# Optimization experiments

Measured on AMD Instinct MI355X. Metric: run time of the kernel, lower is better.

## Reference

```python
import jax, jax.numpy as jnp
import numpy as np

COORD = 5.0
NOOBJ = 0.5
S = 14
B = 2
C = 20
BATCH = 4096


def setup_inputs() -> dict:
    key = jax.random.key(0)
    k1, k2, k3 = jax.random.split(key, 3)
    inp = jax.random.uniform(k1, (BATCH, S, S, 5 * B + C), dtype=jnp.float32)
    tgt = jax.random.uniform(k2, (BATCH, S, S, 5 * B + C), dtype=jnp.float32)
    # target confidence channels must be exactly 0/1 for the obj test
    conf = (jax.random.uniform(k3, (BATCH, S, S, B)) < 0.2).astype(jnp.float32)
    tgt = tgt.at[..., :B].set(conf)
    return {"input": inp, "target": tgt}


def reference(input, target) -> jnp.ndarray:
    n = input.shape[0]
    conf_p = input[..., :B]                      # [N,S,S,B]
    conf_t = target[..., :B]
    box_p = input[..., B:5 * B].reshape(*input.shape[:-1], B, 4)   # [N,S,S,B,4]
    box_t = target[..., B:5 * B].reshape(*target.shape[:-1], B, 4)
    cls_p = input[..., 5 * B:]                   # [N,S,S,C]
    cls_t = target[..., 5 * B:]

    obj = conf_t == 1.0                          # [N,S,S,B]
    has_obj = jnp.any(obj, axis=-1)              # [N,S,S]
    # first responsible box per cell (the original breaks at first k with obj==1)
    first = obj & (jnp.cumsum(obj.astype(jnp.int32), axis=-1) == 1)  # [N,S,S,B]
    firstf = first.astype(input.dtype)

    sq_xy = jnp.sum((box_p[..., :2] - box_t[..., :2]) ** 2, axis=-1)               # [N,S,S,B]
    sq_wh = jnp.sum((jnp.sqrt(box_p[..., 2:]) - jnp.sqrt(box_t[..., 2:])) ** 2, axis=-1)
    sq_conf = (conf_p - conf_t) ** 2                                               # [N,S,S,B]

    loss_xy = jnp.sum(firstf * sq_xy)
    loss_wh = jnp.sum(firstf * sq_wh)
    loss_objc = jnp.sum(firstf * sq_conf)
    # class loss counted once per cell containing an object
    loss_cls = jnp.sum(has_obj.astype(input.dtype) * jnp.sum((cls_p - cls_t) ** 2, axis=-1))
    # no-object: all B confidences in cells with no responsible box
    noobj_mask = (~has_obj).astype(input.dtype)[..., None]
    loss_noobjc = jnp.sum(noobj_mask * sq_conf)

    total = COORD * (loss_xy + loss_wh) + NOOBJ * loss_noobjc + loss_objc + loss_cls
    return total / n
```

## Files before the change

### kernel.cpp

```cpp
#include <hip/hip_runtime.h>


#define COORD 5.0f
#define NOOBJ 0.5f

#define NCELLS   (4096 * 14 * 14)
#define CPC      128
#define CHB      (CPC * 120)
#define NCHUNKS  (NCELLS / CPC)
#define GRID     512
#define THREADS  128

__device__ __forceinline__ float d2f(float a, float b) { float d = a - b; return d * d; }
__device__ __forceinline__ float sqd(float a, float b) {
    return a + b - 2.0f * sqrtf(a * b);
}

__global__ __launch_bounds__(THREADS) void yolo_loss_kernel(
    const float* __restrict__ inp,
    const float* __restrict__ tgt,
    float* __restrict__ out,
    float inv_n)
{
    __shared__ __align__(16) char smem[2][2][CHB];
    __shared__ float wsum[2];

    const int tid  = threadIdx.x;
    const int lane = tid & 63;
    const int wid  = tid >> 6;

    const char* gsrc0 = (const char*)(wid == 0 ? inp : tgt) + (size_t)lane * 16;

    auto stage = [&](int b, int c) {
        const char* g = gsrc0 + (size_t)c * CHB;
        char* l = &smem[b][wid][0];
#pragma unroll
        for (int k = 0; k < 15; ++k) {
            __builtin_amdgcn_global_load_lds(
                (const __attribute__((address_space(1))) void*)(g + k * 1024),
                (__attribute__((address_space(3))) void*)(l + k * 1024), 16, 0, 0);
        }
    };

    float acc = 0.0f;
    int c = blockIdx.x;
    stage(0, c);
    int buf = 0;

    const int half = lane & 1;

    for (; c < NCHUNKS; c += GRID) {
        const int cn = c + GRID;
        if (cn < NCHUNKS) {
            stage(buf ^ 1, cn);
            asm volatile("s_waitcnt vmcnt(15)" ::: "memory");
        } else {
            asm volatile("s_waitcnt vmcnt(0)" ::: "memory");
        }
        asm volatile("s_barrier" ::: "memory");

        const float* li = (const float*)&smem[buf][0][0];
        const float* lt = (const float*)&smem[buf][1][0];

#pragma unroll
        for (int pass = 0; pass < 2; ++pass) {
            const int p = (lane >> 1) + 32 * pass + 64 * wid;
            const int base = 15 * lane + 960 * pass + 1920 * wid;
            const float* ip = li + base;
            const float* tp = lt + base;

            float t0 = lt[p * 30];
            float t1 = lt[p * 30 + 1];
            bool o0 = (t0 == 1.0f), o1 = (t1 == 1.0f);
            float f0 = o0 ? 1.0f : 0.0f;
            float f1 = (o1 && !o0) ? 1.0f : 0.0f;
            float h  = (o0 || o1) ? 1.0f : 0.0f;
            float nf = 1.0f - h;

            if (half == 0) {
                float s0  = d2f(ip[0], tp[0]);
                float s1  = d2f(ip[1], tp[1]);
                float xy0 = d2f(ip[2], tp[2]) + d2f(ip[3], tp[3]);
                float wh0 = sqd(ip[4], tp[4]) + sqd(ip[5], tp[5]);
                float xy1 = d2f(ip[6], tp[6]) + d2f(ip[7], tp[7]);
                float wh1 = sqd(ip[8], tp[8]) + sqd(ip[9], tp[9]);
                float cls = d2f(ip[10], tp[10]) + d2f(ip[11], tp[11]) + d2f(ip[12], tp[12])
                          + d2f(ip[13], tp[13]) + d2f(ip[14], tp[14]);
                acc += COORD * (f0 * (xy0 + wh0) + f1 * (xy1 + wh1))
                     + f0 * s0 + f1 * s1
                     + NOOBJ * nf * (s0 + s1)
                     + h * cls;
            } else {
                float cls = 0.0f;
#pragma unroll
                for (int j = 0; j < 15; ++j)
                    cls += d2f(ip[j], tp[j]);
                acc += h * cls;
            }
        }

        asm volatile("s_barrier" ::: "memory");
        buf ^= 1;
    }

#pragma unroll
    for (int off = 32; off > 0; off >>= 1)
        acc += __shfl_down(acc, off, 64);
    if (lane == 0) wsum[wid] = acc;
    __syncthreads();
    if (tid == 0) atomicAdd(out, (wsum[0] + wsum[1]) * inv_n);
}

extern "C" void kernel_launch(void* const* d_in, const int* in_sizes, int n_in,
                              void* d_out, int out_size, void* d_ws, size_t ws_size,
                              hipStream_t stream) {
    const float* inp = (const float*)d_in[0];
    const float* tgt = (const float*)d_in[1];
    float* out = (float*)d_out;

    hipMemsetAsync(out, 0, sizeof(float), stream);
    yolo_loss_kernel<<<GRID, THREADS, 0, stream>>>(inp, tgt, out, 1.0f / 4096.0f);
}
```

Before: 44.98 us.

## Give each wave its own triple-buffer-free chunk stream with two-deep prefetch and no barriers

```diff
diff --git a/kernel.cpp b/kernel.cpp
--- a/kernel.cpp
+++ b/kernel.cpp
@@ -8,64 +8,69 @@
 #define CPC      128
 #define CHB      (CPC * 120)
 #define NCHUNKS  (NCELLS / CPC)
-#define GRID     512
-#define THREADS  128
+#define NSTREAM  512
 
 __device__ __forceinline__ float d2f(float a, float b) { float d = a - b; return d * d; }
 __device__ __forceinline__ float sqd(float a, float b) {
     return a + b - 2.0f * sqrtf(a * b);
 }
 
-__global__ __launch_bounds__(THREADS) void yolo_loss_kernel(
+__global__ __launch_bounds__(128) void yolo_loss_kernel(
     const float* __restrict__ inp,
     const float* __restrict__ tgt,
     float* __restrict__ out,
     float inv_n)
 {
-    __shared__ __align__(16) char smem[2][2][CHB];
+    __shared__ __align__(16) char smem[2][2][2][CHB];
     __shared__ float wsum[2];
 
     const int tid  = threadIdx.x;
     const int lane = tid & 63;
     const int wid  = tid >> 6;
+    const int wv   = blockIdx.x * 2 + wid;
 
-    const char* gsrc0 = (const char*)(wid == 0 ? inp : tgt) + (size_t)lane * 16;
+    const char* gi0 = (const char*)inp + (size_t)lane * 16;
+    const char* gt0 = (const char*)tgt + (size_t)lane * 16;
 
     auto stage = [&](int b, int c) {
-        const char* g = gsrc0 + (size_t)c * CHB;
-        char* l = &smem[b][wid][0];
+        const char* gi = gi0 + (size_t)c * CHB;
+        const char* gt = gt0 + (size_t)c * CHB;
+        char* li = &smem[wid][b][0][0];
+        char* lt = &smem[wid][b][1][0];
 #pragma unroll
         for (int k = 0; k < 15; ++k) {
             __builtin_amdgcn_global_load_lds(
-                (const __attribute__((address_space(1))) void*)(g + k * 1024),
-                (__attribute__((address_space(3))) void*)(l + k * 1024), 16, 0, 0);
+                (const __attribute__((address_space(1))) void*)(gi + k * 1024),
+                (__attribute__((address_space(3))) void*)(li + k * 1024), 16, 0, 0);
+            __builtin_amdgcn_global_load_lds(
+                (const __attribute__((address_space(1))) void*)(gt + k * 1024),
+                (__attribute__((address_space(3))) void*)(lt + k * 1024), 16, 0, 0);
         }
     };
 
     float acc = 0.0f;
-    int c = blockIdx.x;
+    int c = wv;
     stage(0, c);
-    int buf = 0;
+    stage(1, c + NSTREAM);
+    int cur = 0;
 
     const int half = lane & 1;
 
-    for (; c < NCHUNKS; c += GRID) {
-        const int cn = c + GRID;
-        if (cn < NCHUNKS) {
-            stage(buf ^ 1, cn);
-            asm volatile("s_waitcnt vmcnt(15)" ::: "memory");
+    for (; c < NCHUNKS; c += NSTREAM) {
+        const int cpre = c + 2 * NSTREAM;
+        if (cpre < NCHUNKS) {
+            asm volatile("s_waitcnt vmcnt(30)" ::: "memory");
         } else {
             asm volatile("s_waitcnt vmcnt(0)" ::: "memory");
         }
-        asm volatile("s_barrier" ::: "memory");
 
-        const float* li = (const float*)&smem[buf][0][0];
-        const float* lt = (const float*)&smem[buf][1][0];
+        const float* li = (const float*)&smem[wid][cur][0][0];
+        const float* lt = (const float*)&smem[wid][cur][1][0];
 
 #pragma unroll
-        for (int pass = 0; pass < 2; ++pass) {
-            const int p = (lane >> 1) + 32 * pass + 64 * wid;
-            const int base = 15 * lane + 960 * pass + 1920 * wid;
+        for (int pass = 0; pass < 4; ++pass) {
+            const int p    = (lane >> 1) + 32 * pass;
+            const int base = 15 * lane + 960 * pass;
             const float* ip = li + base;
             const float* tp = lt + base;
 
@@ -99,8 +104,9 @@
             }
         }
 
-        asm volatile("s_barrier" ::: "memory");
-        buf ^= 1;
+        asm volatile("s_waitcnt lgkmcnt(0)" ::: "memory");
+        if (cpre < NCHUNKS) stage(cur, cpre);
+        cur ^= 1;
     }
 
 #pragma unroll
@@ -119,5 +125,5 @@
     float* out = (float*)d_out;
 
     hipMemsetAsync(out, 0, sizeof(float), stream);
-    yolo_loss_kernel<<<GRID, THREADS, 0, stream>>>(inp, tgt, out, 1.0f / 4096.0f);
+    yolo_loss_kernel<<<256, 128, 0, stream>>>(inp, tgt, out, 1.0f / 4096.0f);
 }
```

Result: slower. 58.80 us (+30.7%).
